# Performance work log

Measured on AMD Instinct MI355X. Metric: run time of the kernel, lower is better.

## Reference

```python
import jax, jax.numpy as jnp
import numpy as np

N_NODES = 50000
N_EDGES = 800000
NODE = 128
EDGE = 16
H = 96
OUT = 64
L = 3
BN_EPS = 1e-5


def setup_inputs() -> dict:
    key = jax.random.key(0)
    ks = iter(jax.random.split(key, 48))
    def rn(shape, s=0.05):
        return jax.random.normal(next(ks), shape, dtype=jnp.float32) * s
    inp = {
        "x": jax.random.normal(next(ks), (N_NODES, NODE), dtype=jnp.float32),
        "edge_index": jax.random.randint(next(ks), (2, N_EDGES), 0, N_NODES, dtype=jnp.int32),
        "edge_attr": jax.random.normal(next(ks), (N_EDGES, EDGE), dtype=jnp.float32),
        # GCNConv (layer 0)
        "gcn_lin_w": rn((NODE, H)), "gcn_lin_b": rn((H,)),
        "gcn_root": rn((1, H)),
        "gcn_bw1": rn((EDGE, H)), "gcn_bb1": rn((H,)),
        "gcn_bw2": rn((H, H)), "gcn_bb2": rn((H,)),
        # GINConv layers 1..L-1 (stacked)
        "gin_bw1": rn((L - 1, EDGE, H)), "gin_bb1": rn((L - 1, H)),
        "gin_bw2": rn((L - 1, H, H)), "gin_bb2": rn((L - 1, H)),
        "gin_mw1": rn((L - 1, H, H)), "gin_mb1": rn((L - 1, H)),
        "gin_mw2": rn((L - 1, H, H)), "gin_mb2": rn((L - 1, H)),
        "gin_eps": jnp.zeros((L - 1,), jnp.float32),
        # BatchNorm (eval mode, running stats)
        "bn_gamma": jnp.ones((L, H), jnp.float32),
        "bn_beta": jnp.zeros((L, H), jnp.float32),
        "bn_mean": rn((L, H)),
        "bn_var": jnp.ones((L, H), jnp.float32) + jax.random.uniform(next(ks), (L, H), dtype=jnp.float32) * 0.1,
        # head
        "fc1_w": rn((L * H, H)), "fc1_b": rn((H,)),
        "fc2_w": rn((H, OUT)), "fc2_b": rn((OUT,)),
    }
    return inp


def _bn(x, gamma, beta, mean, var):
    return (x - mean) * jax.lax.rsqrt(var + BN_EPS) * gamma + beta


def reference(x, edge_index, edge_attr,
              gcn_lin_w, gcn_lin_b, gcn_root, gcn_bw1, gcn_bb1, gcn_bw2, gcn_bb2,
              gin_bw1, gin_bb1, gin_bw2, gin_bb2, gin_mw1, gin_mb1, gin_mw2, gin_mb2, gin_eps,
              bn_gamma, bn_beta, bn_mean, bn_var,
              fc1_w, fc1_b, fc2_w, fc2_b):
    n = x.shape[0]
    row, col = edge_index[0], edge_index[1]  # source, target

    # ---- Layer 0: GCNConv with edge attributes ----
    h = x @ gcn_lin_w + gcn_lin_b                                    # [N,H]
    ee = jax.nn.relu(edge_attr @ gcn_bw1 + gcn_bb1) @ gcn_bw2 + gcn_bb2  # [E,H]
    deg = jax.ops.segment_sum(jnp.ones_like(row, dtype=h.dtype), row, num_segments=n) + 1.0
    dinv = jax.lax.rsqrt(deg)                                        # deg >= 1, no inf
    norm = dinv[row] * dinv[col]                                     # [E]
    msg = norm[:, None] * jax.nn.relu(h[row] + ee)                   # [E,H]
    agg = jax.ops.segment_sum(msg, col, num_segments=n)              # [N,H]
    h = agg + jax.nn.relu(h + gcn_root) / deg[:, None]
    h = _bn(jax.nn.relu(h), bn_gamma[0], bn_beta[0], bn_mean[0], bn_var[0])
    feats = [h]

    # ---- Layers 1..L-1: GINConv with edge attributes ----
    for i in range(L - 1):
        ee = jax.nn.relu(edge_attr @ gin_bw1[i] + gin_bb1[i]) @ gin_bw2[i] + gin_bb2[i]  # [E,H]
        agg = jax.ops.segment_sum(jax.nn.relu(h[row] + ee), col, num_segments=n)          # [N,H]
        z = (1.0 + gin_eps[i]) * h + agg
        z = jax.nn.relu(z @ gin_mw1[i] + gin_mb1[i]) @ gin_mw2[i] + gin_mb2[i]
        h = _bn(jax.nn.relu(z), bn_gamma[i + 1], bn_beta[i + 1], bn_mean[i + 1], bn_var[i + 1])
        feats.append(h)

    cat = jnp.concatenate(feats, axis=-1)                            # [N, L*H]
    y = jax.nn.relu(cat @ fc1_w + fc1_b)                             # dropout is eval-mode identity
    return y @ fc2_w + fc2_b                                         # [N, OUT]
```

## Files before the change

### kernel.cpp

```cpp
#include <hip/hip_runtime.h>
#include <hip/hip_bf16.h>


#define HH 96
#define EDGEF 16
#define CAT (3 * HH)

typedef __attribute__((ext_vector_type(8))) short bf16x8;
typedef __attribute__((ext_vector_type(4))) float f32x4;
typedef __attribute__((ext_vector_type(4))) unsigned short ubf16x4;

typedef union { bf16x8 v; unsigned u[4]; } bfpack8;
typedef union { ubf16x4 v; unsigned u[2]; } bfpack4;

__device__ __forceinline__ unsigned short f2bf(float f) {
    unsigned u = __float_as_uint(f);
    u += 0x7fffu + ((u >> 16) & 1u);
    return (unsigned short)(u >> 16);
}
__device__ __forceinline__ float bf2f(unsigned short s) {
    return __uint_as_float(((unsigned)s) << 16);
}
__device__ __forceinline__ unsigned pkbf2(float lo, float hi) {
    __hip_bfloat162 b = __float22bfloat162_rn(make_float2(lo, hi));
    union { __hip_bfloat162 b2; unsigned u; } cv; cv.b2 = b; return cv.u;
}

template <int K, int F, int AMODE, int EPI>
__global__ __launch_bounds__(256) void node_gemm(
    const void* __restrict__ Aptr, int lda,
    const float* __restrict__ agg,
    const float* __restrict__ eps_arr, int li,
    const float* __restrict__ W, const float* __restrict__ bias,
    void* __restrict__ Cptr, int ldc,
    unsigned short* __restrict__ bf_copy,
    const float* __restrict__ gamma, const float* __restrict__ beta,
    const float* __restrict__ mean, const float* __restrict__ var,
    int M)
{
    constexpr int SW = ((K * 2) % 128 == 0) ? 7 : 3;
    constexpr int NFT = F / 16;
    __shared__ __align__(16) short s_wt[F * K];

    const int tid = threadIdx.x;
    const int lane = tid & 63;
    const int w = tid >> 6;
    const int lr = lane & 15;
    const int lg = lane >> 4;

    for (int idx = tid; idx < F * K; idx += 256) {
        int f = idx / K, k = idx - f * K;
        s_wt[idx ^ ((f & SW) << 3)] = (short)f2bf(W[k * F + f]);
    }
    __syncthreads();

    const int R0 = blockIdx.x * 64 + 16 * w;
    const int Ra = min(R0 + lr, M - 1);

    float e1 = 0.f;
    if (AMODE == 2) e1 = 1.f + eps_arr[li];

    f32x4 acc[NFT];
#pragma unroll
    for (int ft = 0; ft < NFT; ++ft) {
        float b = bias[16 * ft + lr];
        acc[ft][0] = b; acc[ft][1] = b; acc[ft][2] = b; acc[ft][3] = b;
    }

#pragma unroll
    for (int kt = 0; kt < K / 32; ++kt) {
        bf16x8 ae;
        if (AMODE == 0) {
            const float* ap = (const float*)Aptr + (size_t)Ra * lda + 32 * kt + 8 * lg;
            f32x4 a0 = *(const f32x4*)ap;
            f32x4 a1 = *(const f32x4*)(ap + 4);
            bfpack8 p;
            p.u[0] = pkbf2(a0[0], a0[1]); p.u[1] = pkbf2(a0[2], a0[3]);
            p.u[2] = pkbf2(a1[0], a1[1]); p.u[3] = pkbf2(a1[2], a1[3]);
            ae = p.v;
        } else if (AMODE == 1) {
            ae = *(const bf16x8*)((const unsigned short*)Aptr + (size_t)Ra * lda + 32 * kt + 8 * lg);
        } else {
            const unsigned short* hp = (const unsigned short*)Aptr + (size_t)Ra * lda + 32 * kt + 8 * lg;
            bf16x8 h8 = *(const bf16x8*)hp;
            const float* gp = agg + (size_t)Ra * HH + 32 * kt + 8 * lg;
            f32x4 g0 = *(const f32x4*)gp;
            f32x4 g1 = *(const f32x4*)(gp + 4);
            float t0 = fmaf(e1, bf2f((unsigned short)h8[0]), g0[0]);
            float t1 = fmaf(e1, bf2f((unsigned short)h8[1]), g0[1]);
            float t2 = fmaf(e1, bf2f((unsigned short)h8[2]), g0[2]);
            float t3 = fmaf(e1, bf2f((unsigned short)h8[3]), g0[3]);
            float t4 = fmaf(e1, bf2f((unsigned short)h8[4]), g1[0]);
            float t5 = fmaf(e1, bf2f((unsigned short)h8[5]), g1[1]);
            float t6 = fmaf(e1, bf2f((unsigned short)h8[6]), g1[2]);
            float t7 = fmaf(e1, bf2f((unsigned short)h8[7]), g1[3]);
            bfpack8 p;
            p.u[0] = pkbf2(t0, t1); p.u[1] = pkbf2(t2, t3);
            p.u[2] = pkbf2(t4, t5); p.u[3] = pkbf2(t6, t7);
            ae = p.v;
        }
#pragma unroll
        for (int ft = 0; ft < NFT; ++ft) {
            bf16x8 bw = *(const bf16x8*)&s_wt[((lr + 16 * ft) * K + 32 * kt + 8 * lg) ^ ((lr & SW) << 3)];
            acc[ft] = __builtin_amdgcn_mfma_f32_16x16x32_bf16(ae, bw, acc[ft], 0, 0, 0);
        }
    }

    float scale[NFT], shiftv[NFT];
    if (EPI == 2) {
#pragma unroll
        for (int ft = 0; ft < NFT; ++ft) {
            int col = 16 * ft + lr;
            float s = gamma[col] * rsqrtf(var[col] + 1e-5f);
            scale[ft] = s;
            shiftv[ft] = beta[col] - mean[col] * s;
        }
    }
#pragma unroll
    for (int reg = 0; reg < 4; ++reg) {
        int r = R0 + 4 * lg + reg;
        if (r < M) {
#pragma unroll
            for (int ft = 0; ft < NFT; ++ft) {
                int col = 16 * ft + lr;
                float v = acc[ft][reg];
                if (EPI == 0) {
                    ((float*)Cptr)[(size_t)r * ldc + col] = v;
                } else if (EPI == 1) {
                    ((unsigned short*)Cptr)[(size_t)r * ldc + col] = f2bf(fmaxf(v, 0.f));
                } else if (EPI == 2) {
                    float z = fmaxf(v, 0.f) * scale[ft] + shiftv[ft];
                    unsigned short zb = f2bf(z);
                    ((unsigned short*)Cptr)[(size_t)r * ldc + col] = zb;
                    bf_copy[(size_t)r * F + col] = zb;
                } else {
                    ((float*)Cptr)[(size_t)r * ldc + col] = v;
                    bf_copy[(size_t)r * F + col] = f2bf(v);
                }
            }
        }
    }
}

__global__ void init_kernel(float* __restrict__ deg, int* __restrict__ cnt, int N)
{
    int i = blockIdx.x * blockDim.x + threadIdx.x;
    if (i < N) { deg[i] = 1.f; cnt[i] = 0; }
}

__global__ void count_kernel(const int* __restrict__ row, const int* __restrict__ col,
                             float* __restrict__ deg, int* __restrict__ cnt, int E)
{
    int e = blockIdx.x * blockDim.x + threadIdx.x;
    if (e < E) {
        atomicAdd(&deg[row[e]], 1.f);
        atomicAdd(&cnt[col[e]], 1);
    }
}

__global__ void scan1_kernel(const int* __restrict__ cnt, int* __restrict__ start,
                             int* __restrict__ bsum, int N)
{
    __shared__ int s[256];
    int tid = threadIdx.x;
    int i = blockIdx.x * 256 + tid;
    int v = (i < N) ? cnt[i] : 0;
    s[tid] = v;
    __syncthreads();
#pragma unroll
    for (int off = 1; off < 256; off <<= 1) {
        int t = (tid >= off) ? s[tid - off] : 0;
        __syncthreads();
        s[tid] += t;
        __syncthreads();
    }
    if (i < N) start[i] = s[tid] - v;
    if (tid == 255) bsum[blockIdx.x] = s[255];
}

__global__ void scan2_kernel(int* __restrict__ bsum, int nb)
{
    __shared__ int s[256];
    int tid = threadIdx.x;
    int v = (tid < nb) ? bsum[tid] : 0;
    s[tid] = v;
    __syncthreads();
#pragma unroll
    for (int off = 1; off < 256; off <<= 1) {
        int t = (tid >= off) ? s[tid - off] : 0;
        __syncthreads();
        s[tid] += t;
        __syncthreads();
    }
    if (tid < nb) bsum[tid] = s[tid] - v;
}

__global__ void scan3_kernel(int* __restrict__ start, const int* __restrict__ bsum,
                             int* __restrict__ cursor,
                             const float* __restrict__ deg, float* __restrict__ dinv,
                             int N, int E)
{
    int i = blockIdx.x * blockDim.x + threadIdx.x;
    if (i < N) {
        int f = start[i] + bsum[i >> 8];
        start[i] = f;
        cursor[i] = f;
        dinv[i] = rsqrtf(deg[i]);
    } else if (i == N) {
        start[N] = E;
    }
}

__global__ void scatter_ea_kernel(const int* __restrict__ row, const int* __restrict__ col,
                                  int* __restrict__ cursor,
                                  const float* __restrict__ ea,
                                  int* __restrict__ row_sorted,
                                  unsigned short* __restrict__ eas, int E)
{
    int e = blockIdx.x * blockDim.x + threadIdx.x;
    if (e >= E) return;
    int c = col[e];
    int p = atomicAdd(&cursor[c], 1);
    row_sorted[p] = row[e];
    const float* src = ea + (size_t)e * EDGEF;
    f32x4 v0 = *(const f32x4*)(src);
    f32x4 v1 = *(const f32x4*)(src + 4);
    f32x4 v2 = *(const f32x4*)(src + 8);
    f32x4 v3 = *(const f32x4*)(src + 12);
    bfpack8 o0, o1;
    o0.u[0] = pkbf2(v0[0], v0[1]); o0.u[1] = pkbf2(v0[2], v0[3]);
    o0.u[2] = pkbf2(v1[0], v1[1]); o0.u[3] = pkbf2(v1[2], v1[3]);
    o1.u[0] = pkbf2(v2[0], v2[1]); o1.u[1] = pkbf2(v2[2], v2[3]);
    o1.u[2] = pkbf2(v3[0], v3[1]); o1.u[3] = pkbf2(v3[2], v3[3]);
    *(bf16x8*)(eas + (size_t)p * EDGEF) = o0.v;
    *(bf16x8*)(eas + (size_t)p * EDGEF + 8) = o1.v;
}

template <bool GCN>
__global__ __launch_bounds__(1024, 8) void edge_kernel(
    const unsigned short* __restrict__ ea_sorted,
    const int* __restrict__ row_sorted,
    const int* __restrict__ seg_start,
    const float* __restrict__ bw1, const float* __restrict__ bb1,
    const float* __restrict__ bw2, const float* __restrict__ bb2,
    const unsigned short* __restrict__ hbf,
    const float* __restrict__ dinv,
    float* __restrict__ agg,
    int N)
{
    __shared__ __align__(16) short s_bw2T[96][104];
    __shared__ __align__(16) short s_bw1T[96][16];
    __shared__ __align__(16) short s_t[16][16][104];
    __shared__ float s_bias[192];

    const int tid = threadIdx.x;
    const int lane = tid & 63;
    const int w = tid >> 6;
    const int lr = lane & 15;
    const int lg = lane >> 4;

    for (int idx = tid; idx < HH * HH; idx += 1024) {
        int k = idx / HH, f = idx - k * HH;
        s_bw2T[f][k] = (short)f2bf(bw2[idx]);
    }
    for (int idx = tid; idx < EDGEF * HH; idx += 1024) {
        int k = idx / HH, f = idx - k * HH;
        s_bw1T[f][k] = (short)f2bf(bw1[idx]);
    }
    if (tid < HH) { s_bias[tid] = bb1[tid]; s_bias[HH + tid] = bb2[tid]; }
    __syncthreads();

    const f32x4 zf = {0.f, 0.f, 0.f, 0.f};
    const int nwaves = gridDim.x * 16;

    for (int c = blockIdx.x * 16 + w; c < N; c += nwaves) {
        const int s0 = seg_start[c];
        const int s1 = seg_start[c + 1];
        float dinv_c = GCN ? dinv[c] : 1.f;

        f32x4 acc[6];
#pragma unroll
        for (int ft = 0; ft < 6; ++ft) acc[ft] = zf;

        for (int b = s0; b < s1; b += 16) {
            const int epos = b + lr;
            const bool vld = (epos < s1);
            const int epc = vld ? epos : s0;
            const int r = row_sorted[epc];

            const unsigned short* hrow = hbf + (size_t)r * HH + 24 * lg;
            bf16x8 h0 = *(const bf16x8*)(hrow);
            bf16x8 h1 = *(const bf16x8*)(hrow + 8);
            bf16x8 h2 = *(const bf16x8*)(hrow + 16);

            const float msk = vld ? (GCN ? dinv[r] * dinv_c : 1.f) : 0.f;

            bf16x8 ae;
#pragma unroll
            for (int j = 0; j < 8; ++j) ae[j] = 0;
            if (lg < 2)
                ae = *(const bf16x8*)(ea_sorted + (size_t)epc * EDGEF + 8 * lg);

#pragma unroll
            for (int ft = 0; ft < 6; ++ft) {
                bf16x8 b1;
#pragma unroll
                for (int j = 0; j < 8; ++j) b1[j] = 0;
                if (lg < 2)
                    b1 = *(const bf16x8*)&s_bw1T[lr + 16 * ft][8 * lg];
                f32x4 tacc = __builtin_amdgcn_mfma_f32_16x16x32_bf16(ae, b1, zf, 0, 0, 0);
                float bsv = s_bias[lr + 16 * ft];
                float v0 = fmaxf(tacc[0] + bsv, 0.f);
                float v1 = fmaxf(tacc[1] + bsv, 0.f);
                float v2 = fmaxf(tacc[2] + bsv, 0.f);
                float v3 = fmaxf(tacc[3] + bsv, 0.f);
                unsigned u01 = pkbf2(v0, v1);
                unsigned u23 = pkbf2(v2, v3);
                const int colf = lr + 16 * ft;
                s_t[w][4 * lg + 0][colf] = (short)u01;
                s_t[w][4 * lg + 1][colf] = (short)(u01 >> 16);
                s_t[w][4 * lg + 2][colf] = (short)u23;
                s_t[w][4 * lg + 3][colf] = (short)(u23 >> 16);
            }
            __builtin_amdgcn_wave_barrier();

            bf16x8 bt[3];
#pragma unroll
            for (int kt = 0; kt < 3; ++kt)
                bt[kt] = *(const bf16x8*)&s_t[w][lr][8 * lg + 32 * kt];
            __builtin_amdgcn_wave_barrier();

            *(bf16x8*)&s_t[w][lr][24 * lg]      = h0;
            *(bf16x8*)&s_t[w][lr][24 * lg + 8]  = h1;
            *(bf16x8*)&s_t[w][lr][24 * lg + 16] = h2;
            __builtin_amdgcn_wave_barrier();

#pragma unroll
            for (int ft = 0; ft < 6; ++ft) {
                const int fb = 16 * ft + 4 * lg;
                f32x4 ee = *(const f32x4*)&s_bias[HH + fb];
#pragma unroll
                for (int kt = 0; kt < 3; ++kt) {
                    bf16x8 aw = *(const bf16x8*)&s_bw2T[lr + 16 * ft][8 * lg + 32 * kt];
                    ee = __builtin_amdgcn_mfma_f32_16x16x32_bf16(aw, bt[kt], ee, 0, 0, 0);
                }
                ubf16x4 hv = *(const ubf16x4*)&s_t[w][lr][fb];
#pragma unroll
                for (int reg = 0; reg < 4; ++reg) {
                    float m = fmaxf(bf2f(hv[reg]) + ee[reg], 0.f);
                    acc[ft][reg] = fmaf(m, msk, acc[ft][reg]);
                }
            }
        }

#pragma unroll
        for (int ft = 0; ft < 6; ++ft) {
#pragma unroll
            for (int reg = 0; reg < 4; ++reg) {
                float v = acc[ft][reg];
                v += __shfl_xor(v, 1);
                v += __shfl_xor(v, 2);
                v += __shfl_xor(v, 4);
                v += __shfl_xor(v, 8);
                acc[ft][reg] = v;
            }
        }
        if (lr == 0) {
#pragma unroll
            for (int ft = 0; ft < 6; ++ft)
                *(f32x4*)&agg[(size_t)c * HH + 16 * ft + 4 * lg] = acc[ft];
        }
    }
}

__global__ void gcn_epilogue_kernel(
    const float* __restrict__ agg, const float* __restrict__ hbuf,
    const float* __restrict__ root, const float* __restrict__ deg,
    const float* __restrict__ gamma, const float* __restrict__ beta,
    const float* __restrict__ mean, const float* __restrict__ var,
    unsigned short* __restrict__ featsbf, unsigned short* __restrict__ hb, int N)
{
    int idx = blockIdx.x * blockDim.x + threadIdx.x;
    if (idx >= N * (HH / 4)) return;
    int n = idx / (HH / 4), q = idx - n * (HH / 4);
    int f0 = 4 * q;
    f32x4 a  = *(const f32x4*)&agg[(size_t)n * HH + f0];
    f32x4 h  = *(const f32x4*)&hbuf[(size_t)n * HH + f0];
    f32x4 rt = *(const f32x4*)&root[f0];
    f32x4 gm = *(const f32x4*)&gamma[f0];
    f32x4 bt = *(const f32x4*)&beta[f0];
    f32x4 mn = *(const f32x4*)&mean[f0];
    f32x4 vr = *(const f32x4*)&var[f0];
    float di = 1.f / deg[n];
    float vv[4];
#pragma unroll
    for (int j = 0; j < 4; ++j) {
        float self = fmaxf(h[j] + rt[j], 0.f) * di;
        float v = fmaxf(a[j] + self, 0.f);
        vv[j] = (v - mn[j]) * rsqrtf(vr[j] + 1e-5f) * gm[j] + bt[j];
    }
    bfpack4 o;
    o.u[0] = pkbf2(vv[0], vv[1]);
    o.u[1] = pkbf2(vv[2], vv[3]);
    *(ubf16x4*)&featsbf[(size_t)n * CAT + f0] = o.v;
    *(ubf16x4*)&hb[(size_t)n * HH + f0] = o.v;
}

extern "C" void kernel_launch(void* const* d_in, const int* in_sizes, int n_in,
                              void* d_out, int out_size, void* d_ws, size_t ws_size,
                              hipStream_t stream)
{
    const float* x         = (const float*)d_in[0];
    const int*   eidx      = (const int*)d_in[1];
    const float* edge_attr = (const float*)d_in[2];
    const float* gcn_lin_w = (const float*)d_in[3];
    const float* gcn_lin_b = (const float*)d_in[4];
    const float* gcn_root  = (const float*)d_in[5];
    const float* gcn_bw1   = (const float*)d_in[6];
    const float* gcn_bb1   = (const float*)d_in[7];
    const float* gcn_bw2   = (const float*)d_in[8];
    const float* gcn_bb2   = (const float*)d_in[9];
    const float* gin_bw1   = (const float*)d_in[10];
    const float* gin_bb1   = (const float*)d_in[11];
    const float* gin_bw2   = (const float*)d_in[12];
    const float* gin_bb2   = (const float*)d_in[13];
    const float* gin_mw1   = (const float*)d_in[14];
    const float* gin_mb1   = (const float*)d_in[15];
    const float* gin_mw2   = (const float*)d_in[16];
    const float* gin_mb2   = (const float*)d_in[17];
    const float* gin_eps   = (const float*)d_in[18];
    const float* bn_gamma  = (const float*)d_in[19];
    const float* bn_beta   = (const float*)d_in[20];
    const float* bn_mean   = (const float*)d_in[21];
    const float* bn_var    = (const float*)d_in[22];
    const float* fc1_w     = (const float*)d_in[23];
    const float* fc1_b     = (const float*)d_in[24];
    const float* fc2_w     = (const float*)d_in[25];
    const float* fc2_b     = (const float*)d_in[26];
    float* out = (float*)d_out;

    const int N = in_sizes[0] / 128;
    const int E = in_sizes[1] / 2;
    const int* row = eidx;
    const int* col = eidx + E;

    char* ws = (char*)d_ws;
    float* deg        = (float*)(ws);
    float* dinv       = (float*)(ws + (size_t)256 * 1024);
    int*   seg_start  = (int*)(ws + (size_t)512 * 1024);
    int*   cursor     = (int*)(ws + (size_t)768 * 1024);
    int*   bsum       = (int*)(ws + (size_t)1024 * 1024);
    int*   row_sorted = (int*)(ws + (size_t)1088 * 1024);
    unsigned short* ea_sorted = (unsigned short*)(ws + (size_t)8 * 1024 * 1024);
    unsigned short* hb        = (unsigned short*)(ws + (size_t)34 * 1024 * 1024);
    float* hbuf   = (float*)(ws + (size_t)44 * 1024 * 1024);
    float* agg    = (float*)(ws + (size_t)64 * 1024 * 1024);
    unsigned short* featsbf = (unsigned short*)(ws + (size_t)84 * 1024 * 1024);
    unsigned short* z1bf    = (unsigned short*)(ws + (size_t)113 * 1024 * 1024);
    unsigned short* r1bf    = (unsigned short*)(ws + (size_t)123 * 1024 * 1024);

    const int ew_blocks = 512;
    const int q_grid = (N * (HH / 4) + 255) / 256;
    const int gemm_grid = (N + 63) / 64;
    const int e_grid = (E + 255) / 256;
    const int n_grid = (N + 255) / 256;
    const int nchunks = (N + 255) / 256;

    init_kernel<<<n_grid, 256, 0, stream>>>(deg, cursor, N);
    count_kernel<<<e_grid, 256, 0, stream>>>(row, col, deg, cursor, E);
    scan1_kernel<<<nchunks, 256, 0, stream>>>(cursor, seg_start, bsum, N);
    scan2_kernel<<<1, 256, 0, stream>>>(bsum, nchunks);
    scan3_kernel<<<(N + 256) / 256, 256, 0, stream>>>(seg_start, bsum, cursor, deg, dinv, N, E);
    scatter_ea_kernel<<<e_grid, 256, 0, stream>>>(row, col, cursor, edge_attr,
                                                  row_sorted, ea_sorted, E);

    node_gemm<128, 96, 0, 3><<<gemm_grid, 256, 0, stream>>>(
        x, 128, nullptr, nullptr, 0, gcn_lin_w, gcn_lin_b,
        hbuf, HH, hb, nullptr, nullptr, nullptr, nullptr, N);
    edge_kernel<true><<<ew_blocks, 1024, 0, stream>>>(
        ea_sorted, row_sorted, seg_start,
        gcn_bw1, gcn_bb1, gcn_bw2, gcn_bb2, hb, dinv, agg, N);
    gcn_epilogue_kernel<<<q_grid, 256, 0, stream>>>(
        agg, hbuf, gcn_root, deg, bn_gamma, bn_beta, bn_mean, bn_var, featsbf, hb, N);

    for (int i = 0; i < 2; ++i) {
        edge_kernel<false><<<ew_blocks, 1024, 0, stream>>>(
            ea_sorted, row_sorted, seg_start,
            gin_bw1 + (size_t)i * EDGEF * HH, gin_bb1 + i * HH,
            gin_bw2 + (size_t)i * HH * HH, gin_bb2 + i * HH,
            hb, dinv, agg, N);
        node_gemm<96, 96, 2, 1><<<gemm_grid, 256, 0, stream>>>(
            hb, HH, agg, gin_eps, i,
            gin_mw1 + (size_t)i * HH * HH, gin_mb1 + i * HH,
            z1bf, HH, nullptr, nullptr, nullptr, nullptr, nullptr, N);
        node_gemm<96, 96, 1, 2><<<gemm_grid, 256, 0, stream>>>(
            z1bf, HH, nullptr, nullptr, 0,
            gin_mw2 + (size_t)i * HH * HH, gin_mb2 + i * HH,
            featsbf + (i + 1) * HH, CAT, hb,
            bn_gamma + (i + 1) * HH, bn_beta + (i + 1) * HH,
            bn_mean + (i + 1) * HH, bn_var + (i + 1) * HH, N);
    }

    node_gemm<288, 96, 1, 1><<<gemm_grid, 256, 0, stream>>>(
        featsbf, CAT, nullptr, nullptr, 0, fc1_w, fc1_b,
        r1bf, HH, nullptr, nullptr, nullptr, nullptr, nullptr, N);
    node_gemm<96, 64, 1, 0><<<gemm_grid, 256, 0, stream>>>(
        r1bf, HH, nullptr, nullptr, 0, fc2_w, fc2_b,
        out, 64, nullptr, nullptr, nullptr, nullptr, nullptr, N);
}
```

Before: 717.7 us.

## Shrink edge kernel blocks, hoist bw1 fragments, swap MFMA operands for vector stores

Edge kernel blocks shrink from 1024 to 256 threads, and twice as many blocks are launched. The per-block shared scratch shrinks to match. The first-stage bw1 MFMA fragments now load into registers once, before the node loop, instead of on every edge tile. The MFMA operands are swapped so the bias can be fed in as the accumulator, and results go out as one packed 8-byte LDS store instead of four scalar stores. This costs more per-block weight staging (more blocks each transposing bw2) and extra registers.

```diff
diff --git a/kernel.cpp b/kernel.cpp
--- a/kernel.cpp
+++ b/kernel.cpp
@@ -9,6 +9,7 @@
 typedef __attribute__((ext_vector_type(8))) short bf16x8;
 typedef __attribute__((ext_vector_type(4))) float f32x4;
 typedef __attribute__((ext_vector_type(4))) unsigned short ubf16x4;
+typedef __attribute__((ext_vector_type(2))) unsigned uint2v;
 
 typedef union { bf16x8 v; unsigned u[4]; } bfpack8;
 typedef union { ubf16x4 v; unsigned u[2]; } bfpack4;
@@ -237,7 +238,7 @@
 }
 
 template <bool GCN>
-__global__ __launch_bounds__(1024, 8) void edge_kernel(
+__global__ __launch_bounds__(256, 4) void edge_kernel(
     const unsigned short* __restrict__ ea_sorted,
     const int* __restrict__ row_sorted,
     const int* __restrict__ seg_start,
@@ -250,7 +251,7 @@
 {
     __shared__ __align__(16) short s_bw2T[96][104];
     __shared__ __align__(16) short s_bw1T[96][16];
-    __shared__ __align__(16) short s_t[16][16][104];
+    __shared__ __align__(16) short s_t[4][16][104];
     __shared__ float s_bias[192];
 
     const int tid = threadIdx.x;
@@ -259,28 +260,37 @@
     const int lr = lane & 15;
     const int lg = lane >> 4;
 
-    for (int idx = tid; idx < HH * HH; idx += 1024) {
+    for (int idx = tid; idx < HH * HH; idx += 256) {
         int k = idx / HH, f = idx - k * HH;
         s_bw2T[f][k] = (short)f2bf(bw2[idx]);
     }
-    for (int idx = tid; idx < EDGEF * HH; idx += 1024) {
+    for (int idx = tid; idx < EDGEF * HH; idx += 256) {
         int k = idx / HH, f = idx - k * HH;
         s_bw1T[f][k] = (short)f2bf(bw1[idx]);
     }
     if (tid < HH) { s_bias[tid] = bb1[tid]; s_bias[HH + tid] = bb2[tid]; }
     __syncthreads();
 
-    const f32x4 zf = {0.f, 0.f, 0.f, 0.f};
-    const int nwaves = gridDim.x * 16;
-
-    for (int c = blockIdx.x * 16 + w; c < N; c += nwaves) {
+    bf16x8 bwf[6];
+#pragma unroll
+    for (int ft = 0; ft < 6; ++ft) {
+        bf16x8 z;
+#pragma unroll
+        for (int j = 0; j < 8; ++j) z[j] = 0;
+        if (lg < 2) z = *(const bf16x8*)&s_bw1T[lr + 16 * ft][8 * lg];
+        bwf[ft] = z;
+    }
+
+    const int nwaves = gridDim.x * 4;
+
+    for (int c = blockIdx.x * 4 + w; c < N; c += nwaves) {
         const int s0 = seg_start[c];
         const int s1 = seg_start[c + 1];
-        float dinv_c = GCN ? dinv[c] : 1.f;
+        const float dinv_c = GCN ? dinv[c] : 1.f;
 
         f32x4 acc[6];
 #pragma unroll
-        for (int ft = 0; ft < 6; ++ft) acc[ft] = zf;
+        for (int ft = 0; ft < 6; ++ft) { acc[ft][0]=0.f; acc[ft][1]=0.f; acc[ft][2]=0.f; acc[ft][3]=0.f; }
 
         for (int b = s0; b < s1; b += 16) {
             const int epos = b + lr;
@@ -295,32 +305,20 @@
 
             const float msk = vld ? (GCN ? dinv[r] * dinv_c : 1.f) : 0.f;
 
-            bf16x8 ae;
-#pragma unroll
-            for (int j = 0; j < 8; ++j) ae[j] = 0;
-            if (lg < 2)
-                ae = *(const bf16x8*)(ea_sorted + (size_t)epc * EDGEF + 8 * lg);
+            bf16x8 ae = *(const bf16x8*)(ea_sorted + (size_t)epc * EDGEF + 8 * (lg & 1));
 
 #pragma unroll
             for (int ft = 0; ft < 6; ++ft) {
-                bf16x8 b1;
-#pragma unroll
-                for (int j = 0; j < 8; ++j) b1[j] = 0;
-                if (lg < 2)
-                    b1 = *(const bf16x8*)&s_bw1T[lr + 16 * ft][8 * lg];
-                f32x4 tacc = __builtin_amdgcn_mfma_f32_16x16x32_bf16(ae, b1, zf, 0, 0, 0);
-                float bsv = s_bias[lr + 16 * ft];
-                float v0 = fmaxf(tacc[0] + bsv, 0.f);
-                float v1 = fmaxf(tacc[1] + bsv, 0.f);
-                float v2 = fmaxf(tacc[2] + bsv, 0.f);
-                float v3 = fmaxf(tacc[3] + bsv, 0.f);
-                unsigned u01 = pkbf2(v0, v1);
-                unsigned u23 = pkbf2(v2, v3);
-                const int colf = lr + 16 * ft;
-                s_t[w][4 * lg + 0][colf] = (short)u01;
-                s_t[w][4 * lg + 1][colf] = (short)(u01 >> 16);
-                s_t[w][4 * lg + 2][colf] = (short)u23;
-                s_t[w][4 * lg + 3][colf] = (short)(u23 >> 16);
+                f32x4 ci = *(const f32x4*)&s_bias[16 * ft + 4 * lg];
+                f32x4 t4 = __builtin_amdgcn_mfma_f32_16x16x32_bf16(bwf[ft], ae, ci, 0, 0, 0);
+                float v0 = fmaxf(t4[0], 0.f);
+                float v1 = fmaxf(t4[1], 0.f);
+                float v2 = fmaxf(t4[2], 0.f);
+                float v3 = fmaxf(t4[3], 0.f);
+                uint2v uu;
+                uu[0] = pkbf2(v0, v1);
+                uu[1] = pkbf2(v2, v3);
+                *(uint2v*)&s_t[w][lr][16 * ft + 4 * lg] = uu;
             }
             __builtin_amdgcn_wave_barrier();
 
@@ -459,7 +457,7 @@
     unsigned short* z1bf    = (unsigned short*)(ws + (size_t)113 * 1024 * 1024);
     unsigned short* r1bf    = (unsigned short*)(ws + (size_t)123 * 1024 * 1024);
 
-    const int ew_blocks = 512;
+    const int ew_blocks = 1024;
     const int q_grid = (N * (HH / 4) + 255) / 256;
     const int gemm_grid = (N + 63) / 64;
     const int e_grid = (E + 255) / 256;
@@ -477,14 +475,14 @@
     node_gemm<128, 96, 0, 3><<<gemm_grid, 256, 0, stream>>>(
         x, 128, nullptr, nullptr, 0, gcn_lin_w, gcn_lin_b,
         hbuf, HH, hb, nullptr, nullptr, nullptr, nullptr, N);
-    edge_kernel<true><<<ew_blocks, 1024, 0, stream>>>(
+    edge_kernel<true><<<ew_blocks, 256, 0, stream>>>(
         ea_sorted, row_sorted, seg_start,
         gcn_bw1, gcn_bb1, gcn_bw2, gcn_bb2, hb, dinv, agg, N);
     gcn_epilogue_kernel<<<q_grid, 256, 0, stream>>>(
         agg, hbuf, gcn_root, deg, bn_gamma, bn_beta, bn_mean, bn_var, featsbf, hb, N);
 
     for (int i = 0; i < 2; ++i) {
-        edge_kernel<false><<<ew_blocks, 1024, 0, stream>>>(
+        edge_kernel<false><<<ew_blocks, 256, 0, stream>>>(
             ea_sorted, row_sorted, seg_start,
             gin_bw1 + (size_t)i * EDGEF * HH, gin_bb1 + i * HH,
             gin_bw2 + (size_t)i * HH * HH, gin_bb2 + i * HH,
```

New measurement: 676.1 us. 1.06x faster.
